# Performance work log

Measured on AMD Instinct MI355X. Metric: run time of the kernel, lower is better.

Reference implementation:

```python
import jax, jax.numpy as jnp
import numpy as np

B, M, C_SEED, NSAMPLE = 2, 1024, 512, 16
BASE_RADIUS, HMIN, HMAX = 0.05, -0.02, 0.04
RADII = [BASE_RADIUS * s for s in (0.25, 0.5, 0.75, 1.0)]
EPS = 1e-5


def _bn_relu(x, g, be, m, v):
    # eval-mode BatchNorm2d over channel axis 1, then ReLU
    s = jax.lax.rsqrt(v + EPS) * g
    return jax.nn.relu((x - m[None, :, None, None]) * s[None, :, None, None] + be[None, :, None, None])


def _crop(xyz, feats, rot, local, radius, params):
    # xyz: (B,N,3); feats: (B,C,N); rot: (B,M,3,3); local: (B,M,N,3) point coords in each seed's rotated frame
    W1, b1, g1, be1, m1, v1, W2, b2, g2, be2, m2, v2 = params
    d2 = local[..., 1] ** 2 + local[..., 2] ** 2
    mask = (d2 < radius * radius) & (local[..., 0] > HMIN) & (local[..., 0] < HMAX)
    # cylinder_query semantics: take first NSAMPLE in-cylinder indices (index order), pad with first found
    order = jnp.argsort(jnp.where(mask, 0, 1).astype(jnp.int32), axis=-1)  # stable sort: valid first
    idx = order[..., :NSAMPLE]                                   # (B,M,ns)
    valid = jnp.take_along_axis(mask, idx, axis=-1)
    idx = jnp.where(valid, idx, idx[..., :1])                    # seed itself is always in-cylinder
    g_xyz = jax.vmap(lambda p, i: p[i])(xyz, idx)                # (B,M,ns,3)
    g_xyz = (g_xyz - xyz[:, :, None, :]) / radius                # center + normalize_xyz
    g_xyz = jnp.einsum('bmnd,bmde->bmne', g_xyz, rot)            # rotate_xyz
    g_feat = jax.vmap(lambda f, i: f[:, i])(feats, idx)          # (B,C,M,ns)
    x = jnp.concatenate([g_xyz.transpose(0, 3, 1, 2), g_feat], axis=1)  # (B,3+C,M,ns)
    x = _bn_relu(jnp.einsum('bcmn,oc->bomn', x, W1) + b1[None, :, None, None], g1, be1, m1, v1)
    x = _bn_relu(jnp.einsum('bcmn,oc->bomn', x, W2) + b2[None, :, None, None], g2, be2, m2, v2)
    return jnp.max(x, axis=-1)                                   # (B,256,M) max-pool over neighbors


def setup_inputs() -> dict:
    key = jax.random.key(0)
    ks = jax.random.split(key, 12)
    C1 = 3 + C_SEED
    inp = {
        'seed_xyz': jax.random.uniform(ks[0], (B, M, 3), dtype=jnp.float32),
        'seed_features': jax.random.normal(ks[1], (B, C_SEED, M), dtype=jnp.float32),
        'vp_rot': jax.random.normal(ks[2], (B, M, 3, 3), dtype=jnp.float32),
        'crop_W1': jax.random.normal(ks[3], (4, 256, C1), dtype=jnp.float32) * 0.05,
        'crop_b1': jax.random.normal(ks[4], (4, 256), dtype=jnp.float32) * 0.05,
        'crop_g1': jnp.ones((4, 256), jnp.float32),
        'crop_be1': jnp.zeros((4, 256), jnp.float32),
        'crop_m1': jnp.zeros((4, 256), jnp.float32),
        'crop_v1': jnp.ones((4, 256), jnp.float32),
        'crop_W2': jax.random.normal(ks[5], (4, 256, 256), dtype=jnp.float32) * 0.05,
        'crop_b2': jax.random.normal(ks[6], (4, 256), dtype=jnp.float32) * 0.05,
        'crop_g2': jnp.ones((4, 256), jnp.float32),
        'crop_be2': jnp.zeros((4, 256), jnp.float32),
        'crop_m2': jnp.zeros((4, 256), jnp.float32),
        'crop_v2': jnp.ones((4, 256), jnp.float32),
        'fuse_W': jax.random.normal(ks[7], (256, 1024), dtype=jnp.float32) * 0.05,
        'fuse_b': jax.random.normal(ks[8], (256,), dtype=jnp.float32) * 0.05,
        'gate_W': jax.random.normal(ks[9], (256, 256), dtype=jnp.float32) * 0.05,
        'gate_b': jax.random.normal(ks[10], (256,), dtype=jnp.float32) * 0.05,
        'trans_W': jax.random.normal(ks[11], (256, C_SEED), dtype=jnp.float32) * 0.05,
        'trans_b': jnp.zeros((256,), jnp.float32),
    }
    return inp


def reference(seed_xyz, seed_features, vp_rot, crop_W1, crop_b1, crop_g1, crop_be1, crop_m1, crop_v1,
              crop_W2, crop_b2, crop_g2, crop_be2, crop_m2, crop_v2,
              fuse_W, fuse_b, gate_W, gate_b, trans_W, trans_b):
    # local[b,m,n] = rot[b,m]^T @ (xyz[b,n] - xyz[b,m])  (row-major rot -> diff @ rot)
    diff = seed_xyz[:, None, :, :] - seed_xyz[:, :, None, :]        # (B,M,N,3)
    local = jnp.einsum('bmnd,bmde->bmne', diff, vp_rot)
    outs = []
    for s, radius in enumerate(RADII):
        params = (crop_W1[s], crop_b1[s], crop_g1[s], crop_be1[s], crop_m1[s], crop_v1[s],
                  crop_W2[s], crop_b2[s], crop_g2[s], crop_be2[s], crop_m2[s], crop_v2[s])
        outs.append(_crop(seed_xyz, seed_features, vp_rot, local, radius, params))
    cat = jnp.concatenate(outs, axis=1)                              # (B,1024,M)
    fused = jnp.einsum('bcm,oc->bom', cat, fuse_W) + fuse_b[None, :, None]
    seed_t = jnp.einsum('bcm,oc->bom', seed_features, trans_W) + trans_b[None, :, None]
    gate = jax.nn.sigmoid(jnp.einsum('bcm,oc->bom', seed_t, gate_W) + gate_b[None, :, None])
    return fused + gate * seed_t                                     # (B,256,M)
```

## Files before the change

### kernel.cpp

```cpp
#include <hip/hip_runtime.h>
#include <math.h>

typedef __attribute__((ext_vector_type(8))) short short8;
typedef __attribute__((ext_vector_type(4))) float f32x4;

__device__ __forceinline__ unsigned short bf16_bits(float f) {
  unsigned u = __float_as_uint(f);
  u += 0x7fffu + ((u >> 16) & 1u);
  return (unsigned short)(u >> 16);
}

__device__ __forceinline__ void gload_lds16(const unsigned short* gp, unsigned short* lp) {
  __builtin_amdgcn_global_load_lds(
      (const __attribute__((address_space(1))) unsigned int*)gp,
      (__attribute__((address_space(3))) unsigned int*)lp, 16, 0, 0);
}

__global__ __launch_bounds__(256) void k0b_prep(
    const float* __restrict__ W1, const float* __restrict__ b1, const float* __restrict__ g1,
    const float* __restrict__ be1, const float* __restrict__ m1, const float* __restrict__ v1,
    const float* __restrict__ W2, const float* __restrict__ b2, const float* __restrict__ g2,
    const float* __restrict__ be2, const float* __restrict__ m2, const float* __restrict__ v2,
    unsigned short* __restrict__ W2f, float4* __restrict__ xyzb,
    float* __restrict__ bias2c, float* __restrict__ s1arr) {
  const int so = blockIdx.x;
  const int j  = threadIdx.x;
  const int s = so >> 8, o = so & 255;
  const float s2 = rsqrtf(v2[so] + 1e-5f) * g2[so];
  const int t = o >> 4, r = o & 15;
  const int ks = j >> 5, hi = (j >> 3) & 3, i = j & 7;
  const int l = hi * 16 + r;
  W2f[(size_t)s * 65536 + (size_t)((ks * 16 + t) << 9) + l * 8 + i] =
      bf16_bits(W2[(size_t)so * 256 + j] * s2);
  if (j == 0) {
    const float s1 = rsqrtf(v1[so] + 1e-5f) * g1[so];
    const float* wr = W1 + (size_t)so * 515;
    xyzb[so] = make_float4(wr[0] * s1, wr[1] * s1, wr[2] * s1,
                           (b1[so] - m1[so]) * s1 + be1[so]);
    bias2c[so] = (b2[so] - m2[so]) * s2 + be2[so];
    s1arr[so] = s1;
  }
}

__global__ __launch_bounds__(256) void k0_neighbors(
    const float* __restrict__ xyz, const float* __restrict__ rot,
    int* __restrict__ idx_arr, float4* __restrict__ gxyz4) {
  const int wid = threadIdx.x >> 6, lane = threadIdx.x & 63;
  const int gw = blockIdx.x * 4 + wid;
  const int b = gw >> 10, m = gw & 1023;
  const float* pm = xyz + (size_t)(b * 1024 + m) * 3;
  const float cx = pm[0], cy = pm[1], cz = pm[2];
  const float* pr = rot + (size_t)(b * 1024 + m) * 9;
  float R[9];
#pragma unroll
  for (int i = 0; i < 9; ++i) R[i] = pr[i];
  const float radf[4] = {0.0125f, 0.025f, 0.0375f, 0.05f};
  const float rad2[4] = {(float)(0.0125 * 0.0125), (float)(0.025 * 0.025),
                         (float)(0.0375 * 0.0375), (float)(0.05 * 0.05)};
  int cnt[4] = {0, 0, 0, 0};
  int firstn[4] = {0, 0, 0, 0};
  float f0x[4] = {0, 0, 0, 0}, f0y[4] = {0, 0, 0, 0}, f0z[4] = {0, 0, 0, 0};
  for (int n0 = 0; n0 < 1024; n0 += 64) {
    const int n = n0 + lane;
    const float* pn = xyz + (size_t)(b * 1024 + n) * 3;
    const float dx = pn[0] - cx, dy = pn[1] - cy, dz = pn[2] - cz;
    const float l0 = dx * R[0] + dy * R[3] + dz * R[6];
    const float l1 = dx * R[1] + dy * R[4] + dz * R[7];
    const float l2 = dx * R[2] + dy * R[5] + dz * R[8];
    const float d2 = l1 * l1 + l2 * l2;
    const bool hok = (l0 > -0.02f) && (l0 < 0.04f);
#pragma unroll
    for (int s = 0; s < 4; ++s) {
      if (cnt[s] >= 16) continue;
      const bool p = hok && (d2 < rad2[s]);
      const unsigned long long bal = __ballot(p);
      if (bal == 0ull) continue;
      if (cnt[s] == 0) {
        const int src = __builtin_ctzll(bal);
        firstn[s] = n0 + src;
        f0x[s] = __shfl(l0, src);
        f0y[s] = __shfl(l1, src);
        f0z[s] = __shfl(l2, src);
      }
      const int rank = __popcll(bal & ((1ull << lane) - 1ull));
      const int slot = cnt[s] + rank;
      if (p && slot < 16) {
        const size_t base = ((size_t)((s * 2 + b) * 1024 + m)) * 16 + slot;
        idx_arr[base] = n;
        gxyz4[base] = make_float4(l0 / radf[s], l1 / radf[s], l2 / radf[s], 0.f);
      }
      cnt[s] = min(cnt[s] + (int)__popcll(bal), 16);
    }
  }
#pragma unroll
  for (int s = 0; s < 4; ++s) {
    if (lane < 16 && lane >= cnt[s]) {
      const size_t base = ((size_t)((s * 2 + b) * 1024 + m)) * 16 + lane;
      idx_arr[base] = firstn[s];
      gxyz4[base] = make_float4(f0x[s] / radf[s], f0y[s] / radf[s], f0z[s] / radf[s], 0.f);
    }
  }
}

__global__ __launch_bounds__(256) void k1_f1(
    const float* __restrict__ feats, const float* __restrict__ W1,
    const float* __restrict__ s1arr, float* __restrict__ F1) {
  __shared__ float At[16][68];
  __shared__ float Bt[16][68];
  const int bid = blockIdx.x;
  const int ogt = bid & 15, nt = (bid >> 4) & 15, b = bid >> 8;
  const int og0 = ogt * 64, n0 = nt * 64;
  const int tx = threadIdx.x & 15, ty = threadIdx.x >> 4;
  float acc[4][4] = {};
  for (int c0 = 0; c0 < 512; c0 += 16) {
#pragma unroll
    for (int it = 0; it < 4; ++it) {
      const int t = threadIdx.x + it * 256;
      { const int cc = t >> 6, nn = t & 63;
        At[cc][nn] = feats[((size_t)(b * 512 + c0 + cc)) * 1024 + n0 + nn]; }
      { const int cc = t & 15, nn = t >> 4;
        const int og = og0 + nn;
        Bt[cc][nn] = W1[(size_t)og * 515 + 3 + c0 + cc] * s1arr[og]; }
    }
    __syncthreads();
#pragma unroll
    for (int cc = 0; cc < 16; ++cc) {
      const float4 a = *(const float4*)&At[cc][ty * 4];
      const float4 bv = *(const float4*)&Bt[cc][tx * 4];
      const float av[4] = {a.x, a.y, a.z, a.w};
      const float bw[4] = {bv.x, bv.y, bv.z, bv.w};
#pragma unroll
      for (int i = 0; i < 4; ++i)
#pragma unroll
        for (int j = 0; j < 4; ++j) acc[i][j] = fmaf(av[i], bw[j], acc[i][j]);
    }
    __syncthreads();
  }
  const int s = og0 >> 8;
  const int obase = (og0 & 255) + tx * 4;
#pragma unroll
  for (int i = 0; i < 4; ++i) {
    const int n = n0 + ty * 4 + i;
    float4 w;
    w.x = acc[i][0]; w.y = acc[i][1]; w.z = acc[i][2]; w.w = acc[i][3];
    *(float4*)&F1[(((size_t)(s * 2 + b)) * 1024 + n) * 256 + obase] = w;
  }
}

__global__ __launch_bounds__(256) void k2_layer2(
    const int* __restrict__ idx_arr, const float4* __restrict__ gxyz4,
    const float* __restrict__ F1, const unsigned short* __restrict__ W2f,
    const float4* __restrict__ xyzb, const float* __restrict__ bias2c,
    float* __restrict__ cat) {
  __shared__ unsigned short sbuf[2][8192];
  const int wid = threadIdx.x >> 6, lane = threadIdx.x & 63;
  const int bid = blockIdx.x;
  const int mg = bid & 255, b = (bid >> 8) & 1, s = bid >> 9;
  const int m = mg * 4 + wid;
  const int r = lane & 15, hi = lane >> 4;
  const size_t sb = (size_t)((s * 2 + b) * 1024 + m) * 16 + r;
  const int n = idx_arr[sb];
  const float4 g = gxyz4[sb];
  const float* __restrict__ f1row = F1 + ((size_t)((s * 2 + b) * 1024) + n) * 256;
  const unsigned short* __restrict__ w2f = W2f + (size_t)s * 65536;
  const float4* __restrict__ xbs = xyzb + s * 256;

  float4 pf[16];
#pragma unroll
  for (int ks = 0; ks < 8; ++ks) {
    const int j0 = ks * 32 + hi * 8;
    pf[ks * 2]     = *(const float4*)(f1row + j0);
    pf[ks * 2 + 1] = *(const float4*)(f1row + j0 + 4);
  }

#pragma unroll
  for (int tt = 0; tt < 4; ++tt) {
    const int t = wid * 4 + tt;
    gload_lds16(w2f + ((size_t)t << 9) + lane * 8, &sbuf[0][t * 512]);
  }
  __syncthreads();

  f32x4 acc[16];
#pragma unroll
  for (int t = 0; t < 16; ++t) { acc[t][0] = 0.f; acc[t][1] = 0.f; acc[t][2] = 0.f; acc[t][3] = 0.f; }

#pragma unroll
  for (int ks = 0; ks < 8; ++ks) {
    const int cur = ks & 1;
    if (ks < 7) {
#pragma unroll
      for (int tt = 0; tt < 4; ++tt) {
        const int t = wid * 4 + tt;
        gload_lds16(w2f + ((size_t)((ks + 1) * 16 + t) << 9) + lane * 8,
                    &sbuf[cur ^ 1][t * 512]);
      }
    }
    const int j0 = ks * 32 + hi * 8;
    const float4 fa = pf[ks * 2], fb = pf[ks * 2 + 1];
    const float fv[8] = {fa.x, fa.y, fa.z, fa.w, fb.x, fb.y, fb.z, fb.w};
    short8 af;
#pragma unroll
    for (int i = 0; i < 8; ++i) {
      const float4 xb = xbs[j0 + i];
      float v = fv[i] + xb.w;
      v = fmaf(g.x, xb.x, v);
      v = fmaf(g.y, xb.y, v);
      v = fmaf(g.z, xb.z, v);
      v = fmaxf(v, 0.f);
      af[i] = (short)bf16_bits(v);
    }
#pragma unroll
    for (int t = 0; t < 16; ++t) {
      const short8 bfv = *(const short8*)&sbuf[cur][t * 512 + lane * 8];
      acc[t] = __builtin_amdgcn_mfma_f32_16x16x32_bf16(af, bfv, acc[t], 0, 0, 0);
    }
    __syncthreads();
  }

  float* __restrict__ catrow = cat + ((size_t)(b * 1024 + m)) * 1024 + s * 256;
#pragma unroll
  for (int t = 0; t < 16; ++t) {
    const float bc = bias2c[s * 256 + t * 16 + r];
    float mv = fmaxf(acc[t][0] + bc, 0.f);
    mv = fmaxf(mv, fmaxf(acc[t][1] + bc, 0.f));
    mv = fmaxf(mv, fmaxf(acc[t][2] + bc, 0.f));
    mv = fmaxf(mv, fmaxf(acc[t][3] + bc, 0.f));
    mv = fmaxf(mv, __shfl_xor(mv, 16));
    mv = fmaxf(mv, __shfl_xor(mv, 32));
    if (hi == 0) catrow[t * 16 + r] = mv;
  }
}

__global__ __launch_bounds__(256) void k3_trans(
    const float* __restrict__ feats, const float* __restrict__ W,
    const float* __restrict__ bias, float* __restrict__ outp) {
  __shared__ float At[16][68];
  __shared__ float Bt[16][68];
  const int bid = blockIdx.x;
  const int ot = bid & 3, nt = (bid >> 2) & 15, b = bid >> 6;
  const int og0 = ot * 64, m0 = nt * 64;
  const int tx = threadIdx.x & 15, ty = threadIdx.x >> 4;
  float acc[4][4] = {};
  for (int c0 = 0; c0 < 512; c0 += 16) {
#pragma unroll
    for (int it = 0; it < 4; ++it) {
      const int t = threadIdx.x + it * 256;
      { const int cc = t >> 6, nn = t & 63;
        At[cc][nn] = feats[((size_t)(b * 512 + c0 + cc)) * 1024 + m0 + nn]; }
      { const int cc = t & 15, nn = t >> 4;
        Bt[cc][nn] = W[(size_t)(og0 + nn) * 512 + c0 + cc]; }
    }
    __syncthreads();
#pragma unroll
    for (int cc = 0; cc < 16; ++cc) {
      const float4 a = *(const float4*)&At[cc][ty * 4];
      const float4 bv = *(const float4*)&Bt[cc][tx * 4];
      const float av[4] = {a.x, a.y, a.z, a.w};
      const float bw[4] = {bv.x, bv.y, bv.z, bv.w};
#pragma unroll
      for (int i = 0; i < 4; ++i)
#pragma unroll
        for (int j = 0; j < 4; ++j) acc[i][j] = fmaf(av[i], bw[j], acc[i][j]);
    }
    __syncthreads();
  }
#pragma unroll
  for (int j = 0; j < 4; ++j) {
    const int og = og0 + tx * 4 + j;
    const float bb = bias[og];
#pragma unroll
    for (int i = 0; i < 4; ++i)
      outp[((size_t)(b * 256 + og)) * 1024 + m0 + ty * 4 + i] = acc[i][j] + bb;
  }
}

__global__ __launch_bounds__(256) void k3_fuse(
    const float* __restrict__ cat, const float* __restrict__ W,
    const float* __restrict__ bias, float* __restrict__ outp) {
  __shared__ float At[16][68];
  __shared__ float Bt[16][68];
  const int bid = blockIdx.x;
  const int ot = bid & 3, nt = (bid >> 2) & 15, b = bid >> 6;
  const int og0 = ot * 64, m0 = nt * 64;
  const int tx = threadIdx.x & 15, ty = threadIdx.x >> 4;
  float acc[4][4] = {};
  for (int c0 = 0; c0 < 1024; c0 += 16) {
#pragma unroll
    for (int it = 0; it < 4; ++it) {
      const int t = threadIdx.x + it * 256;
      { const int mm = t >> 4, cj = t & 15;
        At[cj][mm] = cat[((size_t)(b * 1024 + m0 + mm)) * 1024 + c0 + cj]; }
      { const int cc = t & 15, nn = t >> 4;
        Bt[cc][nn] = W[(size_t)(og0 + nn) * 1024 + c0 + cc]; }
    }
    __syncthreads();
#pragma unroll
    for (int cc = 0; cc < 16; ++cc) {
      const float4 a = *(const float4*)&At[cc][ty * 4];
      const float4 bv = *(const float4*)&Bt[cc][tx * 4];
      const float av[4] = {a.x, a.y, a.z, a.w};
      const float bw[4] = {bv.x, bv.y, bv.z, bv.w};
#pragma unroll
      for (int i = 0; i < 4; ++i)
#pragma unroll
        for (int j = 0; j < 4; ++j) acc[i][j] = fmaf(av[i], bw[j], acc[i][j]);
    }
    __syncthreads();
  }
#pragma unroll
  for (int j = 0; j < 4; ++j) {
    const int og = og0 + tx * 4 + j;
    const float bb = bias[og];
#pragma unroll
    for (int i = 0; i < 4; ++i)
      outp[((size_t)(b * 256 + og)) * 1024 + m0 + ty * 4 + i] = acc[i][j] + bb;
  }
}

__global__ __launch_bounds__(256) void k3_gate(
    const float* __restrict__ seedt, const float* __restrict__ W,
    const float* __restrict__ bias, const float* __restrict__ fused,
    float* __restrict__ outp) {
  __shared__ float At[16][68];
  __shared__ float Bt[16][68];
  const int bid = blockIdx.x;
  const int ot = bid & 3, nt = (bid >> 2) & 15, b = bid >> 6;
  const int og0 = ot * 64, m0 = nt * 64;
  const int tx = threadIdx.x & 15, ty = threadIdx.x >> 4;
  float acc[4][4] = {};
  for (int c0 = 0; c0 < 256; c0 += 16) {
#pragma unroll
    for (int it = 0; it < 4; ++it) {
      const int t = threadIdx.x + it * 256;
      { const int cc = t >> 6, nn = t & 63;
        At[cc][nn] = seedt[((size_t)(b * 256 + c0 + cc)) * 1024 + m0 + nn]; }
      { const int cc = t & 15, nn = t >> 4;
        Bt[cc][nn] = W[(size_t)(og0 + nn) * 256 + c0 + cc]; }
    }
    __syncthreads();
#pragma unroll
    for (int cc = 0; cc < 16; ++cc) {
      const float4 a = *(const float4*)&At[cc][ty * 4];
      const float4 bv = *(const float4*)&Bt[cc][tx * 4];
      const float av[4] = {a.x, a.y, a.z, a.w};
      const float bw[4] = {bv.x, bv.y, bv.z, bv.w};
#pragma unroll
      for (int i = 0; i < 4; ++i)
#pragma unroll
        for (int j = 0; j < 4; ++j) acc[i][j] = fmaf(av[i], bw[j], acc[i][j]);
    }
    __syncthreads();
  }
#pragma unroll
  for (int j = 0; j < 4; ++j) {
    const int og = og0 + tx * 4 + j;
    const float gb = bias[og];
#pragma unroll
    for (int i = 0; i < 4; ++i) {
      const size_t oidx = ((size_t)(b * 256 + og)) * 1024 + m0 + ty * 4 + i;
      const float a = acc[i][j] + gb;
      const float gv = 1.f / (1.f + expf(-a));
      outp[oidx] = fused[oidx] + gv * seedt[oidx];
    }
  }
}

extern "C" void kernel_launch(void* const* d_in, const int* in_sizes, int n_in,
                              void* d_out, int out_size, void* d_ws, size_t ws_size,
                              hipStream_t stream) {
  (void)in_sizes; (void)n_in; (void)out_size; (void)ws_size;
  const float* seed_xyz  = (const float*)d_in[0];
  const float* seed_feat = (const float*)d_in[1];
  const float* vp_rot    = (const float*)d_in[2];
  const float* cW1  = (const float*)d_in[3];
  const float* cb1  = (const float*)d_in[4];
  const float* cg1  = (const float*)d_in[5];
  const float* cbe1 = (const float*)d_in[6];
  const float* cm1  = (const float*)d_in[7];
  const float* cv1  = (const float*)d_in[8];
  const float* cW2  = (const float*)d_in[9];
  const float* cb2  = (const float*)d_in[10];
  const float* cg2  = (const float*)d_in[11];
  const float* cbe2 = (const float*)d_in[12];
  const float* cm2  = (const float*)d_in[13];
  const float* cv2  = (const float*)d_in[14];
  const float* fuse_W  = (const float*)d_in[15];
  const float* fuse_b  = (const float*)d_in[16];
  const float* gate_W  = (const float*)d_in[17];
  const float* gate_b  = (const float*)d_in[18];
  const float* trans_W = (const float*)d_in[19];
  const float* trans_b = (const float*)d_in[20];

  char* ws = (char*)d_ws;
  float4* gxyz4        = (float4*)(ws + 0);
  float4* xyzb         = (float4*)(ws + 2097152);
  float* F1            = (float*)(ws + 2113536);
  float* cat           = (float*)(ws + 10502144);
  float* seedt         = (float*)(ws + 18890752);
  float* fusedb        = (float*)(ws + 20987904);
  int* idx_arr         = (int*)(ws + 23085056);
  unsigned short* W2f  = (unsigned short*)(ws + 23609344);
  float* bias2c        = (float*)(ws + 24133632);
  float* s1arr         = (float*)(ws + 24137728);

  hipLaunchKernelGGL(k0b_prep, dim3(1024), dim3(256), 0, stream,
                     cW1, cb1, cg1, cbe1, cm1, cv1, cW2, cb2, cg2, cbe2, cm2, cv2,
                     W2f, xyzb, bias2c, s1arr);
  hipLaunchKernelGGL(k0_neighbors, dim3(512), dim3(256), 0, stream,
                     seed_xyz, vp_rot, idx_arr, gxyz4);
  hipLaunchKernelGGL(k1_f1, dim3(512), dim3(256), 0, stream,
                     seed_feat, cW1, s1arr, F1);
  hipLaunchKernelGGL(k2_layer2, dim3(2048), dim3(256), 0, stream,
                     idx_arr, gxyz4, F1, W2f, xyzb, bias2c, cat);
  hipLaunchKernelGGL(k3_trans, dim3(128), dim3(256), 0, stream,
                     seed_feat, trans_W, trans_b, seedt);
  hipLaunchKernelGGL(k3_fuse, dim3(128), dim3(256), 0, stream,
                     cat, fuse_W, fuse_b, fusedb);
  hipLaunchKernelGGL(k3_gate, dim3(128), dim3(256), 0, stream,
                     seedt, gate_W, gate_b, fusedb, (float*)d_out);
}
```

Measured before the change: 311.1 us.

## Load layer-2 weights directly into registers and halve output tiles in final GEMMs

The layer-2 MFMA kernel no longer stages W2 through double-buffered LDS with global_load_lds and barriers. Each wave now loads its bf16 weight fragments straight from global memory (L2-resident) into registers every k-step. This removes the synchronisation but raises register pressure and global traffic. Separately, the trans, fuse and gate GEMM kernels move to 32-wide output tiles with 2x4 per-thread accumulators, doubling the grid from 128 to 256 blocks so more CUs are occupied.

```diff
diff --git a/kernel.cpp b/kernel.cpp
--- a/kernel.cpp
+++ b/kernel.cpp
@@ -8,12 +8,6 @@
   unsigned u = __float_as_uint(f);
   u += 0x7fffu + ((u >> 16) & 1u);
   return (unsigned short)(u >> 16);
-}
-
-__device__ __forceinline__ void gload_lds16(const unsigned short* gp, unsigned short* lp) {
-  __builtin_amdgcn_global_load_lds(
-      (const __attribute__((address_space(1))) unsigned int*)gp,
-      (__attribute__((address_space(3))) unsigned int*)lp, 16, 0, 0);
 }
 
 __global__ __launch_bounds__(256) void k0b_prep(
@@ -152,7 +146,6 @@
     const float* __restrict__ F1, const unsigned short* __restrict__ W2f,
     const float4* __restrict__ xyzb, const float* __restrict__ bias2c,
     float* __restrict__ cat) {
-  __shared__ unsigned short sbuf[2][8192];
   const int wid = threadIdx.x >> 6, lane = threadIdx.x & 63;
   const int bid = blockIdx.x;
   const int mg = bid & 255, b = (bid >> 8) & 1, s = bid >> 9;
@@ -173,28 +166,17 @@
     pf[ks * 2 + 1] = *(const float4*)(f1row + j0 + 4);
   }
 
-#pragma unroll
-  for (int tt = 0; tt < 4; ++tt) {
-    const int t = wid * 4 + tt;
-    gload_lds16(w2f + ((size_t)t << 9) + lane * 8, &sbuf[0][t * 512]);
-  }
-  __syncthreads();
-
   f32x4 acc[16];
 #pragma unroll
   for (int t = 0; t < 16; ++t) { acc[t][0] = 0.f; acc[t][1] = 0.f; acc[t][2] = 0.f; acc[t][3] = 0.f; }
 
 #pragma unroll
   for (int ks = 0; ks < 8; ++ks) {
-    const int cur = ks & 1;
-    if (ks < 7) {
-#pragma unroll
-      for (int tt = 0; tt < 4; ++tt) {
-        const int t = wid * 4 + tt;
-        gload_lds16(w2f + ((size_t)((ks + 1) * 16 + t) << 9) + lane * 8,
-                    &sbuf[cur ^ 1][t * 512]);
-      }
-    }
+    const unsigned short* wk = w2f + ((size_t)(ks * 16) << 9) + lane * 8;
+    short8 bf[16];
+#pragma unroll
+    for (int t = 0; t < 16; ++t)
+      bf[t] = *(const short8*)(wk + ((size_t)t << 9));
     const int j0 = ks * 32 + hi * 8;
     const float4 fa = pf[ks * 2], fb = pf[ks * 2 + 1];
     const float fv[8] = {fa.x, fa.y, fa.z, fa.w, fb.x, fb.y, fb.z, fb.w};
@@ -210,11 +192,8 @@
       af[i] = (short)bf16_bits(v);
     }
 #pragma unroll
-    for (int t = 0; t < 16; ++t) {
-      const short8 bfv = *(const short8*)&sbuf[cur][t * 512 + lane * 8];
-      acc[t] = __builtin_amdgcn_mfma_f32_16x16x32_bf16(af, bfv, acc[t], 0, 0, 0);
-    }
-    __syncthreads();
+    for (int t = 0; t < 16; ++t)
+      acc[t] = __builtin_amdgcn_mfma_f32_16x16x32_bf16(af, bf[t], acc[t], 0, 0, 0);
   }
 
   float* __restrict__ catrow = cat + ((size_t)(b * 1024 + m)) * 1024 + s * 256;
@@ -231,34 +210,39 @@
   }
 }
 
+
 __global__ __launch_bounds__(256) void k3_trans(
     const float* __restrict__ feats, const float* __restrict__ W,
     const float* __restrict__ bias, float* __restrict__ outp) {
   __shared__ float At[16][68];
-  __shared__ float Bt[16][68];
+  __shared__ float Bt[16][36];
   const int bid = blockIdx.x;
-  const int ot = bid & 3, nt = (bid >> 2) & 15, b = bid >> 6;
-  const int og0 = ot * 64, m0 = nt * 64;
-  const int tx = threadIdx.x & 15, ty = threadIdx.x >> 4;
-  float acc[4][4] = {};
+  const int ot = bid & 7, nt = (bid >> 3) & 15, b = bid >> 7;
+  const int og0 = ot * 32, m0 = nt * 64;
+  const int tx = threadIdx.x & 7, ty = threadIdx.x >> 3;
+  float acc[2][4] = {};
   for (int c0 = 0; c0 < 512; c0 += 16) {
 #pragma unroll
     for (int it = 0; it < 4; ++it) {
       const int t = threadIdx.x + it * 256;
-      { const int cc = t >> 6, nn = t & 63;
-        At[cc][nn] = feats[((size_t)(b * 512 + c0 + cc)) * 1024 + m0 + nn]; }
-      { const int cc = t & 15, nn = t >> 4;
-        Bt[cc][nn] = W[(size_t)(og0 + nn) * 512 + c0 + cc]; }
+      const int cc = t >> 6, nn = t & 63;
+      At[cc][nn] = feats[((size_t)(b * 512 + c0 + cc)) * 1024 + m0 + nn];
+    }
+#pragma unroll
+    for (int it = 0; it < 2; ++it) {
+      const int t = threadIdx.x + it * 256;
+      const int cc = t & 15, nn = t >> 4;
+      Bt[cc][nn] = W[(size_t)(og0 + nn) * 512 + c0 + cc];
     }
     __syncthreads();
 #pragma unroll
     for (int cc = 0; cc < 16; ++cc) {
-      const float4 a = *(const float4*)&At[cc][ty * 4];
+      const float2 a = *(const float2*)&At[cc][ty * 2];
       const float4 bv = *(const float4*)&Bt[cc][tx * 4];
-      const float av[4] = {a.x, a.y, a.z, a.w};
+      const float av[2] = {a.x, a.y};
       const float bw[4] = {bv.x, bv.y, bv.z, bv.w};
 #pragma unroll
-      for (int i = 0; i < 4; ++i)
+      for (int i = 0; i < 2; ++i)
 #pragma unroll
         for (int j = 0; j < 4; ++j) acc[i][j] = fmaf(av[i], bw[j], acc[i][j]);
     }
@@ -269,8 +253,8 @@
     const int og = og0 + tx * 4 + j;
     const float bb = bias[og];
 #pragma unroll
-    for (int i = 0; i < 4; ++i)
-      outp[((size_t)(b * 256 + og)) * 1024 + m0 + ty * 4 + i] = acc[i][j] + bb;
+    for (int i = 0; i < 2; ++i)
+      outp[((size_t)(b * 256 + og)) * 1024 + m0 + ty * 2 + i] = acc[i][j] + bb;
   }
 }
 
@@ -278,30 +262,34 @@
     const float* __restrict__ cat, const float* __restrict__ W,
     const float* __restrict__ bias, float* __restrict__ outp) {
   __shared__ float At[16][68];
-  __shared__ float Bt[16][68];
+  __shared__ float Bt[16][36];
   const int bid = blockIdx.x;
-  const int ot = bid & 3, nt = (bid >> 2) & 15, b = bid >> 6;
-  const int og0 = ot * 64, m0 = nt * 64;
-  const int tx = threadIdx.x & 15, ty = threadIdx.x >> 4;
-  float acc[4][4] = {};
+  const int ot = bid & 7, nt = (bid >> 3) & 15, b = bid >> 7;
+  const int og0 = ot * 32, m0 = nt * 64;
+  const int tx = threadIdx.x & 7, ty = threadIdx.x >> 3;
+  float acc[2][4] = {};
   for (int c0 = 0; c0 < 1024; c0 += 16) {
 #pragma unroll
     for (int it = 0; it < 4; ++it) {
       const int t = threadIdx.x + it * 256;
-      { const int mm = t >> 4, cj = t & 15;
-        At[cj][mm] = cat[((size_t)(b * 1024 + m0 + mm)) * 1024 + c0 + cj]; }
-      { const int cc = t & 15, nn = t >> 4;
-        Bt[cc][nn] = W[(size_t)(og0 + nn) * 1024 + c0 + cc]; }
+      const int mm = t >> 4, cj = t & 15;
+      At[cj][mm] = cat[((size_t)(b * 1024 + m0 + mm)) * 1024 + c0 + cj];
+    }
+#pragma unroll
+    for (int it = 0; it < 2; ++it) {
+      const int t = threadIdx.x + it * 256;
+      const int cc = t & 15, nn = t >> 4;
+      Bt[cc][nn] = W[(size_t)(og0 + nn) * 1024 + c0 + cc];
     }
     __syncthreads();
 #pragma unroll
     for (int cc = 0; cc < 16; ++cc) {
-      const float4 a = *(const float4*)&At[cc][ty * 4];
+      const float2 a = *(const float2*)&At[cc][ty * 2];
       const float4 bv = *(const float4*)&Bt[cc][tx * 4];
-      const float av[4] = {a.x, a.y, a.z, a.w};
+      const float av[2] = {a.x, a.y};
       const float bw[4] = {bv.x, bv.y, bv.z, bv.w};
 #pragma unroll
-      for (int i = 0; i < 4; ++i)
+      for (int i = 0; i < 2; ++i)
 #pragma unroll
         for (int j = 0; j < 4; ++j) acc[i][j] = fmaf(av[i], bw[j], acc[i][j]);
     }
@@ -312,8 +300,8 @@
     const int og = og0 + tx * 4 + j;
     const float bb = bias[og];
 #pragma unroll
-    for (int i = 0; i < 4; ++i)
-      outp[((size_t)(b * 256 + og)) * 1024 + m0 + ty * 4 + i] = acc[i][j] + bb;
+    for (int i = 0; i < 2; ++i)
+      outp[((size_t)(b * 256 + og)) * 1024 + m0 + ty * 2 + i] = acc[i][j] + bb;
   }
 }
 
@@ -322,30 +310,34 @@
     const float* __restrict__ bias, const float* __restrict__ fused,
     float* __restrict__ outp) {
   __shared__ float At[16][68];
-  __shared__ float Bt[16][68];
+  __shared__ float Bt[16][36];
   const int bid = blockIdx.x;
-  const int ot = bid & 3, nt = (bid >> 2) & 15, b = bid >> 6;
-  const int og0 = ot * 64, m0 = nt * 64;
-  const int tx = threadIdx.x & 15, ty = threadIdx.x >> 4;
-  float acc[4][4] = {};
+  const int ot = bid & 7, nt = (bid >> 3) & 15, b = bid >> 7;
+  const int og0 = ot * 32, m0 = nt * 64;
+  const int tx = threadIdx.x & 7, ty = threadIdx.x >> 3;
+  float acc[2][4] = {};
   for (int c0 = 0; c0 < 256; c0 += 16) {
 #pragma unroll
     for (int it = 0; it < 4; ++it) {
       const int t = threadIdx.x + it * 256;
-      { const int cc = t >> 6, nn = t & 63;
-        At[cc][nn] = seedt[((size_t)(b * 256 + c0 + cc)) * 1024 + m0 + nn]; }
-      { const int cc = t & 15, nn = t >> 4;
-        Bt[cc][nn] = W[(size_t)(og0 + nn) * 256 + c0 + cc]; }
+      const int cc = t >> 6, nn = t & 63;
+      At[cc][nn] = seedt[((size_t)(b * 256 + c0 + cc)) * 1024 + m0 + nn];
+    }
+#pragma unroll
+    for (int it = 0; it < 2; ++it) {
+      const int t = threadIdx.x + it * 256;
+      const int cc = t & 15, nn = t >> 4;
+      Bt[cc][nn] = W[(size_t)(og0 + nn) * 256 + c0 + cc];
     }
     __syncthreads();
 #pragma unroll
     for (int cc = 0; cc < 16; ++cc) {
-      const float4 a = *(const float4*)&At[cc][ty * 4];
+      const float2 a = *(const float2*)&At[cc][ty * 2];
       const float4 bv = *(const float4*)&Bt[cc][tx * 4];
-      const float av[4] = {a.x, a.y, a.z, a.w};
+      const float av[2] = {a.x, a.y};
       const float bw[4] = {bv.x, bv.y, bv.z, bv.w};
 #pragma unroll
-      for (int i = 0; i < 4; ++i)
+      for (int i = 0; i < 2; ++i)
 #pragma unroll
         for (int j = 0; j < 4; ++j) acc[i][j] = fmaf(av[i], bw[j], acc[i][j]);
     }
@@ -356,8 +348,8 @@
     const int og = og0 + tx * 4 + j;
     const float gb = bias[og];
 #pragma unroll
-    for (int i = 0; i < 4; ++i) {
-      const size_t oidx = ((size_t)(b * 256 + og)) * 1024 + m0 + ty * 4 + i;
+    for (int i = 0; i < 2; ++i) {
+      const size_t oidx = ((size_t)(b * 256 + og)) * 1024 + m0 + ty * 2 + i;
       const float a = acc[i][j] + gb;
       const float gv = 1.f / (1.f + expf(-a));
       outp[oidx] = fused[oidx] + gv * seedt[oidx];
@@ -412,10 +404,10 @@
                      seed_feat, cW1, s1arr, F1);
   hipLaunchKernelGGL(k2_layer2, dim3(2048), dim3(256), 0, stream,
                      idx_arr, gxyz4, F1, W2f, xyzb, bias2c, cat);
-  hipLaunchKernelGGL(k3_trans, dim3(128), dim3(256), 0, stream,
+  hipLaunchKernelGGL(k3_trans, dim3(256), dim3(256), 0, stream,
                      seed_feat, trans_W, trans_b, seedt);
-  hipLaunchKernelGGL(k3_fuse, dim3(128), dim3(256), 0, stream,
+  hipLaunchKernelGGL(k3_fuse, dim3(256), dim3(256), 0, stream,
                      cat, fuse_W, fuse_b, fusedb);
-  hipLaunchKernelGGL(k3_gate, dim3(128), dim3(256), 0, stream,
+  hipLaunchKernelGGL(k3_gate, dim3(256), dim3(256), 0, stream,
                      seedt, gate_W, gate_b, fusedb, (float*)d_out);
 }
```

After: 298.5 us. 4.0% less time.
